# Performance work log

Measured on AMD Instinct MI355X. Metric: run time of the kernel, lower is better.

The kernel has to match this reference:

```python
import jax, jax.numpy as jnp
import numpy as np

N, F, H, C, K = 4096, 128, 128, 10, 4  # nodes, feat dim, hidden, classes, num_graphs
EDGE_P = 0.005


def setup_inputs() -> dict:
    key = jax.random.key(0)
    ks = jax.random.split(key, 20)
    feat_matrix = jax.random.normal(ks[0], (N, F), jnp.float32)
    # binary adjacency (dense_to_sparse + GCNConv without edge_weight => weights all 1)
    adj = (jax.random.uniform(ks[1], (N, N, K)) < EDGE_P).astype(jnp.float32)
    adj_matrix = adj * (1.0 - jnp.eye(N, dtype=jnp.float32))[:, :, None]  # no self loops in input
    s = 0.05
    gcn_w1 = jax.random.normal(ks[2], (K, F, H), jnp.float32) * s
    gcn_b1 = jnp.zeros((K, H), jnp.float32)
    gcn_w2 = jax.random.normal(ks[3], (K, H, H), jnp.float32) * s
    gcn_b2 = jnp.zeros((K, H), jnp.float32)
    # PyTorch LSTM params (gate order i,f,g,o), forward and backward directions
    wih_f = jax.random.normal(ks[4], (4 * H, H), jnp.float32) * s
    whh_f = jax.random.normal(ks[5], (4 * H, H), jnp.float32) * s
    bih_f = jnp.zeros((4 * H,), jnp.float32)
    bhh_f = jnp.zeros((4 * H,), jnp.float32)
    wih_b = jax.random.normal(ks[6], (4 * H, H), jnp.float32) * s
    whh_b = jax.random.normal(ks[7], (4 * H, H), jnp.float32) * s
    bih_b = jnp.zeros((4 * H,), jnp.float32)
    bhh_b = jnp.zeros((4 * H,), jnp.float32)
    rnn_out_w = jax.random.normal(ks[8], (1, 2 * H), jnp.float32) * s
    rnn_out_b = jnp.zeros((1,), jnp.float32)
    out_w = jax.random.normal(ks[9], (C, H), jnp.float32) * s
    out_b = jnp.zeros((C,), jnp.float32)
    get_item_index = jnp.arange(N, dtype=jnp.int64)
    set_index = jax.random.randint(ks[10], (1024,), 0, N).astype(jnp.int64)
    val_index = jax.random.randint(ks[11], (1024,), 0, N).astype(jnp.int64)
    mask_matrix = jnp.ones((N,), jnp.bool_)
    return dict(feat_matrix=feat_matrix, adj_matrix=adj_matrix,
                gcn_w1=gcn_w1, gcn_b1=gcn_b1, gcn_w2=gcn_w2, gcn_b2=gcn_b2,
                wih_f=wih_f, whh_f=whh_f, bih_f=bih_f, bhh_f=bhh_f,
                wih_b=wih_b, whh_b=whh_b, bih_b=bih_b, bhh_b=bhh_b,
                rnn_out_w=rnn_out_w, rnn_out_b=rnn_out_b, out_w=out_w, out_b=out_b,
                get_item_index=get_item_index, set_index=set_index,
                val_index=val_index, mask_matrix=mask_matrix)


def _gcn_norm(adj):
    # GCNConv default: A_hat = A + I, sym-normalized D^-1/2 A_hat D^-1/2
    a_hat = adj + jnp.eye(adj.shape[0], dtype=adj.dtype)
    dinv = jax.lax.rsqrt(a_hat.sum(axis=1))
    return dinv[:, None] * a_hat * dinv[None, :]


def _lstm_dir(xs, wih, whh, bih, bhh, reverse):
    # xs: [N, K, H] -> hs: [N, K, H]; scan over the (short) block axis K
    n, h = xs.shape[0], whh.shape[1]
    def step(carry, x_t):
        hp, cp = carry
        g = x_t @ wih.T + hp @ whh.T + (bih + bhh)
        i, f, gg, o = jnp.split(g, 4, axis=-1)
        c = jax.nn.sigmoid(f) * cp + jax.nn.sigmoid(i) * jnp.tanh(gg)
        hn = jax.nn.sigmoid(o) * jnp.tanh(c)
        return (hn, c), hn
    init = (jnp.zeros((n, h), xs.dtype), jnp.zeros((n, h), xs.dtype))
    _, hs = jax.lax.scan(step, init, jnp.swapaxes(xs, 0, 1), reverse=reverse)
    return jnp.swapaxes(hs, 0, 1)


def reference(feat_matrix, adj_matrix, gcn_w1, gcn_b1, gcn_w2, gcn_b2,
              wih_f, whh_f, bih_f, bhh_f, wih_b, whh_b, bih_b, bhh_b,
              rnn_out_w, rnn_out_b, out_w, out_b,
              get_item_index, set_index, val_index, mask_matrix):
    k_blocks = adj_matrix.shape[-1]
    gnn_output = []
    for k in range(k_blocks):  # fixed small number of structurally distinct graph blocks
        an = _gcn_norm(adj_matrix[:, :, k])                 # [N, N]
        h = an @ (feat_matrix @ gcn_w1[k]) + gcn_b1[k]      # GCNConv 1 (no activation)
        h = an @ (h @ gcn_w2[k]) + gcn_b2[k]                # GCNConv 2
        gnn_output.append(h)
    gnn_out = jnp.stack(gnn_output, axis=1)                 # [N, K, H]
    h_fwd = _lstm_dir(gnn_out, wih_f, whh_f, bih_f, bhh_f, reverse=False)
    h_bwd = _lstm_dir(gnn_out, wih_b, whh_b, bih_b, bhh_b, reverse=True)
    rnn_hid = jnp.concatenate([h_fwd, h_bwd], axis=-1)      # [N, K, 2H]
    attn = jax.nn.softmax(rnn_hid @ rnn_out_w.T + rnn_out_b, axis=1)  # [N, K, 1]
    pooled = (gnn_out * attn).sum(axis=1)                   # [N, H]
    return jax.nn.softmax(pooled @ out_w.T + out_b, axis=-1)  # [N, C]
```

## Files before the change

kernel.cpp:

```cpp
#include <hip/hip_runtime.h>
#include <hip/hip_bf16.h>

#define NN 4096
#define HD 128
#define KG 4
#define NC 10
#define CAP 64

typedef __attribute__((ext_vector_type(8))) short bf16x8;
typedef __attribute__((ext_vector_type(4))) float f32x4;

__device__ inline unsigned short f2b(float x) {
    unsigned u = __float_as_uint(x);
    return (unsigned short)((u + 0x7FFFu + ((u >> 16) & 1u)) >> 16);
}
__device__ inline uint2 pack4(float4 v) {
    uint2 p;
    p.x = (unsigned)f2b(v.x) | ((unsigned)f2b(v.y) << 16);
    p.y = (unsigned)f2b(v.z) | ((unsigned)f2b(v.w) << 16);
    return p;
}

__global__ __launch_bounds__(256) void prep_kernel(
    const float* __restrict__ wih_f, const float* __restrict__ whh_f,
    const float* __restrict__ bih_f, const float* __restrict__ bhh_f,
    const float* __restrict__ wih_b, const float* __restrict__ whh_b,
    const float* __restrict__ bih_b, const float* __restrict__ bhh_b,
    const float* __restrict__ gw1, const float* __restrict__ gw2,
    unsigned short* __restrict__ Wp, float* __restrict__ bp,
    unsigned short* __restrict__ Wg1p, unsigned short* __restrict__ Wg2p)
{
    int tid = blockIdx.x * 256 + threadIdx.x;
    if (tid < 2 * 512 * 256) {
        int dir = tid >> 17;
        int rem = tid & 131071;
        int n = rem >> 8, k = rem & 255;
        int tn = n >> 7, wn = (n >> 6) & 1, g = (n >> 4) & 3, c = n & 15;
        int h = tn * 32 + wn * 16 + c;
        int row = g * HD + h;
        const float* wih = dir ? wih_b : wih_f;
        const float* whh = dir ? whh_b : whh_f;
        float v = (k < HD) ? wih[row * HD + k] : whh[row * HD + (k - HD)];
        Wp[tid] = f2b(v);
    } else if (tid < 2 * 512 * 256 + 512 * 128) {
        int t = tid - 2 * 512 * 256;
        int n = t >> 7, k = t & 127;
        int kg = n >> 7, hcol = n & 127;
        Wg1p[t] = f2b(gw1[((size_t)kg * HD + k) * HD + hcol]);
    } else if (tid < 2 * 512 * 256 + 2 * 512 * 128) {
        int t = tid - (2 * 512 * 256 + 512 * 128);
        int n = t >> 7, k = t & 127;
        int kg = n >> 7, hcol = n & 127;
        Wg2p[t] = f2b(gw2[((size_t)kg * HD + k) * HD + hcol]);
    }
    if (tid < 2 * 512) {
        int dir = tid >> 9, n = tid & 511;
        int tn = n >> 7, wn = (n >> 6) & 1, g = (n >> 4) & 3, c = n & 15;
        int h = tn * 32 + wn * 16 + c;
        int row = g * HD + h;
        const float* bih = dir ? bih_b : bih_f;
        const float* bhh = dir ? bhh_b : bhh_f;
        bp[tid] = bih[row] + bhh[row];
    }
}

__global__ __launch_bounds__(256) void extract_kernel(
    const float* __restrict__ adj, float* __restrict__ dinv,
    int* __restrict__ ecnt, unsigned short* __restrict__ edges)
{
    int i = blockIdx.x;
    __shared__ int cnt[KG];
    if (threadIdx.x < KG) cnt[threadIdx.x] = 0;
    __syncthreads();
    const float4* row = (const float4*)(adj + (size_t)i * NN * KG);
    for (int j = threadIdx.x; j < NN; j += 256) {
        float4 v = row[j];
        if (v.x != 0.f) { int p = atomicAdd(&cnt[0], 1); if (p < CAP) edges[((size_t)(0 * NN + i)) * CAP + p] = (unsigned short)j; }
        if (v.y != 0.f) { int p = atomicAdd(&cnt[1], 1); if (p < CAP) edges[((size_t)(1 * NN + i)) * CAP + p] = (unsigned short)j; }
        if (v.z != 0.f) { int p = atomicAdd(&cnt[2], 1); if (p < CAP) edges[((size_t)(2 * NN + i)) * CAP + p] = (unsigned short)j; }
        if (v.w != 0.f) { int p = atomicAdd(&cnt[3], 1); if (p < CAP) edges[((size_t)(3 * NN + i)) * CAP + p] = (unsigned short)j; }
    }
    __syncthreads();
    if (threadIdx.x < KG) {
        int c = cnt[threadIdx.x];
        ecnt[threadIdx.x * NN + i] = c > CAP ? CAP : c;
        dinv[threadIdx.x * NN + i] = rsqrtf((float)c + 1.0f);
    }
}

__device__ inline void stageA(const float* __restrict__ A, int lda, int m0, int kc,
                              unsigned short* Abuf)
{
    int t = threadIdx.x;
#pragma unroll
    for (int it = 0; it < 2; ++it) {
        int f = t + it * 256;
        int r = f >> 3, q = f & 7;
        float4 v = *(const float4*)(A + (size_t)(m0 + r) * lda + kc + (q << 2));
        *(uint2*)&Abuf[r * 40 + q * 4] = pack4(v);
    }
}
__device__ inline void stageB(const unsigned short* __restrict__ Bp, int ldk,
                              int bn0, int kc, unsigned short* Bbuf)
{
    int t = threadIdx.x;
#pragma unroll
    for (int it = 0; it < 2; ++it) {
        int f = t + it * 256;
        int r = f >> 2, q = f & 3;
        uint4 v = *(const uint4*)(Bp + (size_t)(bn0 + r) * ldk + kc + (q << 3));
        *(uint4*)&Bbuf[r * 40 + q * 8] = v;
    }
}
__device__ inline void mfma_chunk(const unsigned short* Abuf, const unsigned short* Bbuf,
                                  int wm, int wn, int lane, f32x4 acc[2][4])
{
    int la = lane & 15, kb = (lane >> 4) * 8;
    bf16x8 a[2], b[4];
#pragma unroll
    for (int m = 0; m < 2; ++m)
        a[m] = *(const bf16x8*)&Abuf[(wm * 32 + m * 16 + la) * 40 + kb];
#pragma unroll
    for (int n = 0; n < 4; ++n)
        b[n] = *(const bf16x8*)&Bbuf[(wn * 64 + n * 16 + la) * 40 + kb];
#pragma unroll
    for (int m = 0; m < 2; ++m)
#pragma unroll
        for (int n = 0; n < 4; ++n)
            acc[m][n] = __builtin_amdgcn_mfma_f32_16x16x32_bf16(a[m], b[n], acc[m][n], 0, 0, 0);
}

__global__ __launch_bounds__(256) void gemm_gcn_mfma(
    const float* __restrict__ Aall, int a_per_k,
    const unsigned short* __restrict__ Bp, float* __restrict__ C)
{
    __shared__ unsigned short Abuf[64 * 40];
    __shared__ unsigned short Bbuf[128 * 40];
    int kg = blockIdx.x;
    int m0 = blockIdx.y * 64;
    const float* A = Aall + (a_per_k ? (size_t)kg * NN * HD : 0);
    int wid = threadIdx.x >> 6, lane = threadIdx.x & 63;
    int wm = wid >> 1, wn = wid & 1;
    f32x4 acc[2][4] = {};
    for (int ch = 0; ch < 4; ++ch) {
        stageA(A, HD, m0, ch * 32, Abuf);
        stageB(Bp, HD, kg * 128, ch * 32, Bbuf);
        __syncthreads();
        mfma_chunk(Abuf, Bbuf, wm, wn, lane, acc);
        __syncthreads();
    }
    float* Cb = C + (size_t)kg * NN * HD;
    int la = lane & 15, lj = lane >> 4;
#pragma unroll
    for (int m = 0; m < 2; ++m)
#pragma unroll
        for (int n = 0; n < 4; ++n)
#pragma unroll
            for (int j = 0; j < 4; ++j) {
                int r = m0 + wm * 32 + m * 16 + lj * 4 + j;
                int col = wn * 64 + n * 16 + la;
                Cb[(size_t)r * HD + col] = acc[m][n][j];
            }
}

__global__ __launch_bounds__(256) void spmm_kernel(
    const float* __restrict__ Z, const float* __restrict__ dinv,
    const int* __restrict__ ecnt, const unsigned short* __restrict__ edges,
    const float* __restrict__ bias, float* __restrict__ Out)
{
    int wid = threadIdx.x >> 6;
    int lane = threadIdx.x & 63;
    int idx = blockIdx.x * 4 + wid;
    int k = idx >> 12;
    int i = idx & (NN - 1);
    int cnt = ecnt[idx];
    float di = dinv[idx];
    const unsigned short* el = edges + (size_t)idx * CAP;
    const float* Zk = Z + (size_t)k * NN * HD;
    int h2 = lane * 2;
    float ax = 0.f, ay = 0.f;
    for (int e = 0; e < cnt; ++e) {
        int j = el[e];
        float dj = dinv[(k << 12) + j];
        float2 z = *(const float2*)(Zk + (size_t)j * HD + h2);
        ax = fmaf(dj, z.x, ax);
        ay = fmaf(dj, z.y, ay);
    }
    float2 zi = *(const float2*)(Zk + (size_t)i * HD + h2);
    ax = fmaf(di, zi.x, ax);
    ay = fmaf(di, zi.y, ay);
    float2 b = *(const float2*)(bias + k * HD + h2);
    float2 o;
    o.x = fmaf(di, ax, b.x);
    o.y = fmaf(di, ay, b.y);
    *(float2*)(Out + (size_t)idx * HD + h2) = o;
}

template <int FIRST>
__global__ __launch_bounds__(256) void lstm_step_mfma(
    const float* __restrict__ gnn, float* __restrict__ hs,
    float* __restrict__ cstate, const unsigned short* __restrict__ Wp,
    const float* __restrict__ bp, int t)
{
    __shared__ unsigned short Abuf[64 * 40];
    __shared__ unsigned short Bbuf[128 * 40];
    int dir = blockIdx.z;
    int kin   = (dir == 0) ? t : (KG - 1 - t);
    int kprev = (dir == 0) ? (t - 1) : (KG - t);
    int bn0 = blockIdx.x * 128;
    int m0  = blockIdx.y * 64;
    int wid = threadIdx.x >> 6, lane = threadIdx.x & 63;
    int wm = wid >> 1, wn = wid & 1;
    const unsigned short* B = Wp + (size_t)dir * 512 * 256;
    const float* A1 = gnn + (size_t)kin * NN * HD;
    const float* A2 = FIRST ? A1 : hs + ((size_t)dir * KG + kprev) * NN * HD;
    f32x4 acc[2][4] = {};
    int nch = FIRST ? 4 : 8;
    for (int ch = 0; ch < nch; ++ch) {
        const float* A = (ch < 4) ? A1 : A2;
        stageA(A, HD, m0, (ch & 3) * 32, Abuf);
        stageB(B, 256, bn0, ch * 32, Bbuf);
        __syncthreads();
        mfma_chunk(Abuf, Bbuf, wm, wn, lane, acc);
        __syncthreads();
    }
    int la = lane & 15, lj = lane >> 4;
    int h = blockIdx.x * 32 + wn * 16 + la;
    const float* bpd = bp + dir * 512;
    float bi = bpd[bn0 + wn * 64 + 0 * 16 + la];
    float bf = bpd[bn0 + wn * 64 + 1 * 16 + la];
    float bg = bpd[bn0 + wn * 64 + 2 * 16 + la];
    float bo = bpd[bn0 + wn * 64 + 3 * 16 + la];
    float* hout = hs + ((size_t)dir * KG + kin) * NN * HD;
    float* cst = cstate + (size_t)dir * NN * HD;
#pragma unroll
    for (int m = 0; m < 2; ++m)
#pragma unroll
        for (int j = 0; j < 4; ++j) {
            int n = m0 + wm * 32 + m * 16 + lj * 4 + j;
            float gi = acc[m][0][j] + bi;
            float gf = acc[m][1][j] + bf;
            float gg = acc[m][2][j] + bg;
            float go = acc[m][3][j] + bo;
            float cold = FIRST ? 0.f : cst[(size_t)n * HD + h];
            float si = 1.f / (1.f + __expf(-gi));
            float sf = 1.f / (1.f + __expf(-gf));
            float so = 1.f / (1.f + __expf(-go));
            float e2g = __expf(2.f * gg);
            float tg = 1.f - 2.f / (e2g + 1.f);
            float cn = fmaf(sf, cold, si * tg);
            float e2c = __expf(2.f * cn);
            float tc = 1.f - 2.f / (e2c + 1.f);
            cst[(size_t)n * HD + h] = cn;
            hout[(size_t)n * HD + h] = so * tc;
        }
}

__global__ __launch_bounds__(256) void finalize_kernel(
    const float* __restrict__ gnn, const float* __restrict__ hs,
    const float* __restrict__ rw, const float* __restrict__ ow,
    const float* __restrict__ ob, float* __restrict__ out)
{
    int wid = threadIdx.x >> 6, lane = threadIdx.x & 63;
    int n = blockIdx.x * 4 + wid;
    float w0 = rw[lane], w1 = rw[lane + 64];
    float w2 = rw[128 + lane], w3 = rw[192 + lane];
    float lg[KG];
#pragma unroll
    for (int k = 0; k < KG; ++k) {
        const float* hf = hs + ((size_t)k * NN + n) * HD;
        const float* hb = hs + ((size_t)(KG + k) * NN + n) * HD;
        lg[k] = hf[lane] * w0 + hf[lane + 64] * w1 + hb[lane] * w2 + hb[lane + 64] * w3;
    }
#pragma unroll
    for (int s = 32; s > 0; s >>= 1)
#pragma unroll
        for (int k = 0; k < KG; ++k) lg[k] += __shfl_xor(lg[k], s);
    float mx = lg[0];
#pragma unroll
    for (int k = 1; k < KG; ++k) mx = fmaxf(mx, lg[k]);
    float es[KG], se = 0.f;
#pragma unroll
    for (int k = 0; k < KG; ++k) { es[k] = __expf(lg[k] - mx); se += es[k]; }
    float inv = 1.f / se;
    float p0 = 0.f, p1 = 0.f;
#pragma unroll
    for (int k = 0; k < KG; ++k) {
        float a = es[k] * inv;
        p0 = fmaf(a, gnn[((size_t)k * NN + n) * HD + lane], p0);
        p1 = fmaf(a, gnn[((size_t)k * NN + n) * HD + lane + 64], p1);
    }
    float oc[NC];
#pragma unroll
    for (int c = 0; c < NC; ++c)
        oc[c] = p0 * ow[c * HD + lane] + p1 * ow[c * HD + lane + 64];
#pragma unroll
    for (int s = 32; s > 0; s >>= 1)
#pragma unroll
        for (int c = 0; c < NC; ++c) oc[c] += __shfl_xor(oc[c], s);
    float omx = oc[0] + ob[0];
#pragma unroll
    for (int c = 0; c < NC; ++c) { oc[c] += ob[c]; omx = fmaxf(omx, oc[c]); }
    float osum = 0.f;
#pragma unroll
    for (int c = 0; c < NC; ++c) { oc[c] = __expf(oc[c] - omx); osum += oc[c]; }
    float oinv = 1.f / osum;
    if (lane < NC) out[(size_t)n * NC + lane] = oc[lane] * oinv;
}

extern "C" void kernel_launch(void* const* d_in, const int* in_sizes, int n_in,
                              void* d_out, int out_size, void* d_ws, size_t ws_size,
                              hipStream_t stream)
{
    const float* feat  = (const float*)d_in[0];
    const float* adj   = (const float*)d_in[1];
    const float* gw1   = (const float*)d_in[2];
    const float* gb1   = (const float*)d_in[3];
    const float* gw2   = (const float*)d_in[4];
    const float* gb2   = (const float*)d_in[5];
    const float* wih_f = (const float*)d_in[6];
    const float* whh_f = (const float*)d_in[7];
    const float* bih_f = (const float*)d_in[8];
    const float* bhh_f = (const float*)d_in[9];
    const float* wih_b = (const float*)d_in[10];
    const float* whh_b = (const float*)d_in[11];
    const float* bih_b = (const float*)d_in[12];
    const float* bhh_b = (const float*)d_in[13];
    const float* rw    = (const float*)d_in[14];
    const float* ow    = (const float*)d_in[16];
    const float* ob    = (const float*)d_in[17];
    float* out = (float*)d_out;

    char* ws = (char*)d_ws;
    float*          dinv  = (float*)(ws);
    int*            ecnt  = (int*)(ws + 65536);
    unsigned short* edges = (unsigned short*)(ws + 131072);
    float*          Z     = (float*)(ws + 2228224);
    float*          G     = (float*)(ws + 10616832);
    float*          hsb   = (float*)(ws + 19005440);
    float*          cst   = (float*)(ws + 35782656);
    unsigned short* Wp    = (unsigned short*)(ws + 39976960);
    float*          bp    = (float*)(ws + 40501248);
    unsigned short* Wg1p  = (unsigned short*)(ws + 40505344);
    unsigned short* Wg2p  = (unsigned short*)(ws + 40636416);

    prep_kernel<<<1536, 256, 0, stream>>>(wih_f, whh_f, bih_f, bhh_f,
                                          wih_b, whh_b, bih_b, bhh_b,
                                          gw1, gw2, Wp, bp, Wg1p, Wg2p);
    extract_kernel<<<NN, 256, 0, stream>>>(adj, dinv, ecnt, edges);
    gemm_gcn_mfma<<<dim3(KG, 64), 256, 0, stream>>>(feat, 0, Wg1p, Z);
    spmm_kernel<<<KG * NN / 4, 256, 0, stream>>>(Z, dinv, ecnt, edges, gb1, G);
    gemm_gcn_mfma<<<dim3(KG, 64), 256, 0, stream>>>(G, 1, Wg2p, Z);
    spmm_kernel<<<KG * NN / 4, 256, 0, stream>>>(Z, dinv, ecnt, edges, gb2, G);
    lstm_step_mfma<1><<<dim3(4, 64, 2), 256, 0, stream>>>(G, hsb, cst, Wp, bp, 0);
    for (int t = 1; t < KG; ++t)
        lstm_step_mfma<0><<<dim3(4, 64, 2), 256, 0, stream>>>(G, hsb, cst, Wp, bp, t);
    finalize_kernel<<<NN / 4, 256, 0, stream>>>(G, hsb, rw, ow, ob, out);
}
```

Before: 548.3 us.

## Fuse setup kernels, emit bf16 intermediates, and fuse LSTM timesteps into one kernel

Merges the prep and adjacency-extraction kernels into one setup launch that also converts features to bf16. The SpMM now writes bf16 copies of its output, so the GEMMs and LSTM load bf16 directly without converting in the inner loop. The four per-timestep LSTM launches become one persistent kernel that keeps the cell state in registers and h in LDS, removing the global c/h round trips and the extra launches. The trade-off is that the LSTM runs on only 128 blocks with a large LDS footprint, and hidden states are stored in bf16, which costs precision.

```diff
diff --git a/kernel.cpp b/kernel.cpp
--- a/kernel.cpp
+++ b/kernel.cpp
@@ -14,143 +14,116 @@
     unsigned u = __float_as_uint(x);
     return (unsigned short)((u + 0x7FFFu + ((u >> 16) & 1u)) >> 16);
 }
-__device__ inline uint2 pack4(float4 v) {
-    uint2 p;
-    p.x = (unsigned)f2b(v.x) | ((unsigned)f2b(v.y) << 16);
-    p.y = (unsigned)f2b(v.z) | ((unsigned)f2b(v.w) << 16);
-    return p;
-}
-
-__global__ __launch_bounds__(256) void prep_kernel(
+__device__ inline float b2f(unsigned short b) {
+    return __uint_as_float((unsigned)b << 16);
+}
+
+__global__ __launch_bounds__(256) void setup_kernel(
+    const float* __restrict__ adj, const float* __restrict__ feat,
     const float* __restrict__ wih_f, const float* __restrict__ whh_f,
     const float* __restrict__ bih_f, const float* __restrict__ bhh_f,
     const float* __restrict__ wih_b, const float* __restrict__ whh_b,
     const float* __restrict__ bih_b, const float* __restrict__ bhh_b,
     const float* __restrict__ gw1, const float* __restrict__ gw2,
+    float* __restrict__ dinv, int* __restrict__ ecnt,
+    unsigned short* __restrict__ edges, unsigned* __restrict__ featb,
     unsigned short* __restrict__ Wp, float* __restrict__ bp,
     unsigned short* __restrict__ Wg1p, unsigned short* __restrict__ Wg2p)
 {
-    int tid = blockIdx.x * 256 + threadIdx.x;
-    if (tid < 2 * 512 * 256) {
-        int dir = tid >> 17;
-        int rem = tid & 131071;
+    int b = blockIdx.x;
+    __shared__ int cnt[KG];
+    if (b < NN) {
+        int i = b;
+        if (threadIdx.x < KG) cnt[threadIdx.x] = 0;
+        __syncthreads();
+        const float4* row = (const float4*)(adj + (size_t)i * NN * KG);
+        for (int j = threadIdx.x; j < NN; j += 256) {
+            float4 v = row[j];
+            if (v.x != 0.f) { int p = atomicAdd(&cnt[0], 1); if (p < CAP) edges[((size_t)(0 * NN + i)) * CAP + p] = (unsigned short)j; }
+            if (v.y != 0.f) { int p = atomicAdd(&cnt[1], 1); if (p < CAP) edges[((size_t)(1 * NN + i)) * CAP + p] = (unsigned short)j; }
+            if (v.z != 0.f) { int p = atomicAdd(&cnt[2], 1); if (p < CAP) edges[((size_t)(2 * NN + i)) * CAP + p] = (unsigned short)j; }
+            if (v.w != 0.f) { int p = atomicAdd(&cnt[3], 1); if (p < CAP) edges[((size_t)(3 * NN + i)) * CAP + p] = (unsigned short)j; }
+        }
+        __syncthreads();
+        if (threadIdx.x < KG) {
+            int c = cnt[threadIdx.x];
+            ecnt[threadIdx.x * NN + i] = c > CAP ? CAP : c;
+            dinv[threadIdx.x * NN + i] = rsqrtf((float)c + 1.0f);
+        }
+    } else if (b < NN + 1024) {
+        int t = (b - NN) * 256 + threadIdx.x;
+        int dir = t >> 17, rem = t & 131071;
         int n = rem >> 8, k = rem & 255;
-        int tn = n >> 7, wn = (n >> 6) & 1, g = (n >> 4) & 3, c = n & 15;
-        int h = tn * 32 + wn * 16 + c;
-        int row = g * HD + h;
+        int hq = n >> 6, g = (n >> 4) & 3, hr = n & 15;
+        int row = g * HD + hq * 16 + hr;
         const float* wih = dir ? wih_b : wih_f;
         const float* whh = dir ? whh_b : whh_f;
-        float v = (k < HD) ? wih[row * HD + k] : whh[row * HD + (k - HD)];
-        Wp[tid] = f2b(v);
-    } else if (tid < 2 * 512 * 256 + 512 * 128) {
-        int t = tid - 2 * 512 * 256;
+        Wp[t] = f2b(k < HD ? wih[row * HD + k] : whh[row * HD + (k - HD)]);
+    } else if (b < NN + 1280) {
+        int t = (b - NN - 1024) * 256 + threadIdx.x;
         int n = t >> 7, k = t & 127;
-        int kg = n >> 7, hcol = n & 127;
-        Wg1p[t] = f2b(gw1[((size_t)kg * HD + k) * HD + hcol]);
-    } else if (tid < 2 * 512 * 256 + 2 * 512 * 128) {
-        int t = tid - (2 * 512 * 256 + 512 * 128);
+        Wg1p[t] = f2b(gw1[(((size_t)(n >> 7)) * HD + k) * HD + (n & 127)]);
+    } else if (b < NN + 1536) {
+        int t = (b - NN - 1280) * 256 + threadIdx.x;
         int n = t >> 7, k = t & 127;
-        int kg = n >> 7, hcol = n & 127;
-        Wg2p[t] = f2b(gw2[((size_t)kg * HD + k) * HD + hcol]);
-    }
-    if (tid < 2 * 512) {
-        int dir = tid >> 9, n = tid & 511;
-        int tn = n >> 7, wn = (n >> 6) & 1, g = (n >> 4) & 3, c = n & 15;
-        int h = tn * 32 + wn * 16 + c;
-        int row = g * HD + h;
-        const float* bih = dir ? bih_b : bih_f;
-        const float* bhh = dir ? bhh_b : bhh_f;
-        bp[tid] = bih[row] + bhh[row];
-    }
-}
-
-__global__ __launch_bounds__(256) void extract_kernel(
-    const float* __restrict__ adj, float* __restrict__ dinv,
-    int* __restrict__ ecnt, unsigned short* __restrict__ edges)
-{
-    int i = blockIdx.x;
-    __shared__ int cnt[KG];
-    if (threadIdx.x < KG) cnt[threadIdx.x] = 0;
-    __syncthreads();
-    const float4* row = (const float4*)(adj + (size_t)i * NN * KG);
-    for (int j = threadIdx.x; j < NN; j += 256) {
-        float4 v = row[j];
-        if (v.x != 0.f) { int p = atomicAdd(&cnt[0], 1); if (p < CAP) edges[((size_t)(0 * NN + i)) * CAP + p] = (unsigned short)j; }
-        if (v.y != 0.f) { int p = atomicAdd(&cnt[1], 1); if (p < CAP) edges[((size_t)(1 * NN + i)) * CAP + p] = (unsigned short)j; }
-        if (v.z != 0.f) { int p = atomicAdd(&cnt[2], 1); if (p < CAP) edges[((size_t)(2 * NN + i)) * CAP + p] = (unsigned short)j; }
-        if (v.w != 0.f) { int p = atomicAdd(&cnt[3], 1); if (p < CAP) edges[((size_t)(3 * NN + i)) * CAP + p] = (unsigned short)j; }
-    }
-    __syncthreads();
-    if (threadIdx.x < KG) {
-        int c = cnt[threadIdx.x];
-        ecnt[threadIdx.x * NN + i] = c > CAP ? CAP : c;
-        dinv[threadIdx.x * NN + i] = rsqrtf((float)c + 1.0f);
-    }
-}
-
-__device__ inline void stageA(const float* __restrict__ A, int lda, int m0, int kc,
-                              unsigned short* Abuf)
-{
-    int t = threadIdx.x;
-#pragma unroll
-    for (int it = 0; it < 2; ++it) {
-        int f = t + it * 256;
-        int r = f >> 3, q = f & 7;
-        float4 v = *(const float4*)(A + (size_t)(m0 + r) * lda + kc + (q << 2));
-        *(uint2*)&Abuf[r * 40 + q * 4] = pack4(v);
-    }
-}
-__device__ inline void stageB(const unsigned short* __restrict__ Bp, int ldk,
-                              int bn0, int kc, unsigned short* Bbuf)
-{
-    int t = threadIdx.x;
-#pragma unroll
-    for (int it = 0; it < 2; ++it) {
-        int f = t + it * 256;
-        int r = f >> 2, q = f & 3;
-        uint4 v = *(const uint4*)(Bp + (size_t)(bn0 + r) * ldk + kc + (q << 3));
-        *(uint4*)&Bbuf[r * 40 + q * 8] = v;
-    }
-}
-__device__ inline void mfma_chunk(const unsigned short* Abuf, const unsigned short* Bbuf,
-                                  int wm, int wn, int lane, f32x4 acc[2][4])
-{
-    int la = lane & 15, kb = (lane >> 4) * 8;
-    bf16x8 a[2], b[4];
-#pragma unroll
-    for (int m = 0; m < 2; ++m)
-        a[m] = *(const bf16x8*)&Abuf[(wm * 32 + m * 16 + la) * 40 + kb];
-#pragma unroll
-    for (int n = 0; n < 4; ++n)
-        b[n] = *(const bf16x8*)&Bbuf[(wn * 64 + n * 16 + la) * 40 + kb];
-#pragma unroll
-    for (int m = 0; m < 2; ++m)
-#pragma unroll
-        for (int n = 0; n < 4; ++n)
-            acc[m][n] = __builtin_amdgcn_mfma_f32_16x16x32_bf16(a[m], b[n], acc[m][n], 0, 0, 0);
+        Wg2p[t] = f2b(gw2[(((size_t)(n >> 7)) * HD + k) * HD + (n & 127)]);
+    } else if (b < NN + 2560) {
+        int t = (b - NN - 1536) * 256 + threadIdx.x;
+        float2 v = *(const float2*)&feat[2 * (size_t)t];
+        featb[t] = (unsigned)f2b(v.x) | ((unsigned)f2b(v.y) << 16);
+    } else {
+        int t = (b - NN - 2560) * 256 + threadIdx.x;
+        if (t < 1024) {
+            int dir = t >> 9, n = t & 511;
+            int hq = n >> 6, g = (n >> 4) & 3, hr = n & 15;
+            int row = g * HD + hq * 16 + hr;
+            bp[t] = dir ? (bih_b[row] + bhh_b[row]) : (bih_f[row] + bhh_f[row]);
+        }
+    }
 }
 
 __global__ __launch_bounds__(256) void gemm_gcn_mfma(
-    const float* __restrict__ Aall, int a_per_k,
+    const unsigned short* __restrict__ Ab, int a_per_k,
     const unsigned short* __restrict__ Bp, float* __restrict__ C)
 {
     __shared__ unsigned short Abuf[64 * 40];
     __shared__ unsigned short Bbuf[128 * 40];
-    int kg = blockIdx.x;
-    int m0 = blockIdx.y * 64;
-    const float* A = Aall + (a_per_k ? (size_t)kg * NN * HD : 0);
+    int kg = blockIdx.x, m0 = blockIdx.y * 64;
+    const unsigned short* A = Ab + (a_per_k ? (size_t)kg * NN * HD : 0);
     int wid = threadIdx.x >> 6, lane = threadIdx.x & 63;
     int wm = wid >> 1, wn = wid & 1;
+    int la = lane & 15, kb = (lane >> 4) * 8;
     f32x4 acc[2][4] = {};
     for (int ch = 0; ch < 4; ++ch) {
-        stageA(A, HD, m0, ch * 32, Abuf);
-        stageB(Bp, HD, kg * 128, ch * 32, Bbuf);
-        __syncthreads();
-        mfma_chunk(Abuf, Bbuf, wm, wn, lane, acc);
+        {
+            int t = threadIdx.x, r = t >> 2, q = t & 3;
+            *(uint4*)&Abuf[r * 40 + q * 8] =
+                *(const uint4*)&A[((size_t)(m0 + r)) * HD + ch * 32 + q * 8];
+        }
+#pragma unroll
+        for (int it = 0; it < 2; ++it) {
+            int f = threadIdx.x + it * 256;
+            int r = f >> 2, q = f & 3;
+            *(uint4*)&Bbuf[r * 40 + q * 8] =
+                *(const uint4*)&Bp[((size_t)(kg * 128 + r)) * HD + ch * 32 + q * 8];
+        }
+        __syncthreads();
+        bf16x8 a[2], bb[4];
+#pragma unroll
+        for (int m = 0; m < 2; ++m)
+            a[m] = *(const bf16x8*)&Abuf[(wm * 32 + m * 16 + la) * 40 + kb];
+#pragma unroll
+        for (int n = 0; n < 4; ++n)
+            bb[n] = *(const bf16x8*)&Bbuf[(wn * 64 + n * 16 + la) * 40 + kb];
+#pragma unroll
+        for (int m = 0; m < 2; ++m)
+#pragma unroll
+            for (int n = 0; n < 4; ++n)
+                acc[m][n] = __builtin_amdgcn_mfma_f32_16x16x32_bf16(a[m], bb[n], acc[m][n], 0, 0, 0);
         __syncthreads();
     }
     float* Cb = C + (size_t)kg * NN * HD;
-    int la = lane & 15, lj = lane >> 4;
+    int lj = lane >> 4;
 #pragma unroll
     for (int m = 0; m < 2; ++m)
 #pragma unroll
@@ -163,10 +136,12 @@
             }
 }
 
+template <int WF32>
 __global__ __launch_bounds__(256) void spmm_kernel(
     const float* __restrict__ Z, const float* __restrict__ dinv,
     const int* __restrict__ ecnt, const unsigned short* __restrict__ edges,
-    const float* __restrict__ bias, float* __restrict__ Out)
+    const float* __restrict__ bias, float* __restrict__ Out,
+    unsigned* __restrict__ Outb)
 {
     int wid = threadIdx.x >> 6;
     int lane = threadIdx.x & 63;
@@ -189,88 +164,116 @@
     float2 zi = *(const float2*)(Zk + (size_t)i * HD + h2);
     ax = fmaf(di, zi.x, ax);
     ay = fmaf(di, zi.y, ay);
-    float2 b = *(const float2*)(bias + k * HD + h2);
+    float2 bv = *(const float2*)(bias + k * HD + h2);
     float2 o;
-    o.x = fmaf(di, ax, b.x);
-    o.y = fmaf(di, ay, b.y);
-    *(float2*)(Out + (size_t)idx * HD + h2) = o;
-}
-
-template <int FIRST>
-__global__ __launch_bounds__(256) void lstm_step_mfma(
-    const float* __restrict__ gnn, float* __restrict__ hs,
-    float* __restrict__ cstate, const unsigned short* __restrict__ Wp,
-    const float* __restrict__ bp, int t)
-{
+    o.x = fmaf(di, ax, bv.x);
+    o.y = fmaf(di, ay, bv.y);
+    if (WF32) *(float2*)(Out + (size_t)idx * HD + h2) = o;
+    Outb[(size_t)idx * 64 + lane] = (unsigned)f2b(o.x) | ((unsigned)f2b(o.y) << 16);
+}
+
+__global__ __launch_bounds__(256) void lstm_fused(
+    const unsigned short* __restrict__ G2b, unsigned short* __restrict__ hsb,
+    const unsigned short* __restrict__ Wp, const float* __restrict__ bp)
+{
+    __shared__ unsigned short Bbuf[512 * 40];
     __shared__ unsigned short Abuf[64 * 40];
-    __shared__ unsigned short Bbuf[128 * 40];
-    int dir = blockIdx.z;
-    int kin   = (dir == 0) ? t : (KG - 1 - t);
-    int kprev = (dir == 0) ? (t - 1) : (KG - t);
-    int bn0 = blockIdx.x * 128;
-    int m0  = blockIdx.y * 64;
+    __shared__ unsigned short hlds[64 * 136];
+    int m0 = blockIdx.x * 64;
+    int dir = blockIdx.y;
     int wid = threadIdx.x >> 6, lane = threadIdx.x & 63;
-    int wm = wid >> 1, wn = wid & 1;
+    int la = lane & 15, lj = lane >> 4, kb = lj * 8;
     const unsigned short* B = Wp + (size_t)dir * 512 * 256;
-    const float* A1 = gnn + (size_t)kin * NN * HD;
-    const float* A2 = FIRST ? A1 : hs + ((size_t)dir * KG + kprev) * NN * HD;
-    f32x4 acc[2][4] = {};
-    int nch = FIRST ? 4 : 8;
-    for (int ch = 0; ch < nch; ++ch) {
-        const float* A = (ch < 4) ? A1 : A2;
-        stageA(A, HD, m0, (ch & 3) * 32, Abuf);
-        stageB(B, 256, bn0, ch * 32, Bbuf);
-        __syncthreads();
-        mfma_chunk(Abuf, Bbuf, wm, wn, lane, acc);
-        __syncthreads();
-    }
-    int la = lane & 15, lj = lane >> 4;
-    int h = blockIdx.x * 32 + wn * 16 + la;
-    const float* bpd = bp + dir * 512;
-    float bi = bpd[bn0 + wn * 64 + 0 * 16 + la];
-    float bf = bpd[bn0 + wn * 64 + 1 * 16 + la];
-    float bg = bpd[bn0 + wn * 64 + 2 * 16 + la];
-    float bo = bpd[bn0 + wn * 64 + 3 * 16 + la];
-    float* hout = hs + ((size_t)dir * KG + kin) * NN * HD;
-    float* cst = cstate + (size_t)dir * NN * HD;
-#pragma unroll
-    for (int m = 0; m < 2; ++m)
-#pragma unroll
-        for (int j = 0; j < 4; ++j) {
-            int n = m0 + wm * 32 + m * 16 + lj * 4 + j;
-            float gi = acc[m][0][j] + bi;
-            float gf = acc[m][1][j] + bf;
-            float gg = acc[m][2][j] + bg;
-            float go = acc[m][3][j] + bo;
-            float cold = FIRST ? 0.f : cst[(size_t)n * HD + h];
-            float si = 1.f / (1.f + __expf(-gi));
-            float sf = 1.f / (1.f + __expf(-gf));
-            float so = 1.f / (1.f + __expf(-go));
-            float e2g = __expf(2.f * gg);
-            float tg = 1.f - 2.f / (e2g + 1.f);
-            float cn = fmaf(sf, cold, si * tg);
-            float e2c = __expf(2.f * cn);
-            float tc = 1.f - 2.f / (e2c + 1.f);
-            cst[(size_t)n * HD + h] = cn;
-            hout[(size_t)n * HD + h] = so * tc;
-        }
+    float c_st[4][2][4] = {};
+    float bias[2][4];
+#pragma unroll
+    for (int ch = 0; ch < 2; ++ch)
+#pragma unroll
+        for (int g = 0; g < 4; ++g)
+            bias[ch][g] = bp[dir * 512 + wid * 128 + (ch * 4 + g) * 16 + la];
+
+    for (int t = 0; t < KG; ++t) {
+        int kin = dir ? (KG - 1 - t) : t;
+        f32x4 acc[4][8] = {};
+        int nch = (t == 0) ? 4 : 8;
+        for (int ch = 0; ch < nch; ++ch) {
+            if (ch < 4) {
+                int r = threadIdx.x >> 2, q = threadIdx.x & 3;
+                *(uint4*)&Abuf[r * 40 + q * 8] =
+                    *(const uint4*)&G2b[((size_t)kin * NN + m0 + r) * HD + ch * 32 + q * 8];
+            }
+#pragma unroll
+            for (int it = 0; it < 8; ++it) {
+                int f = threadIdx.x + it * 256;
+                int r = f >> 2, q = f & 3;
+                *(uint4*)&Bbuf[r * 40 + q * 8] =
+                    *(const uint4*)&B[(size_t)r * 256 + ch * 32 + q * 8];
+            }
+            __syncthreads();
+            bf16x8 bfr[8];
+#pragma unroll
+            for (int fi = 0; fi < 8; ++fi)
+                bfr[fi] = *(const bf16x8*)&Bbuf[(wid * 128 + fi * 16 + la) * 40 + kb];
+#pragma unroll
+            for (int m = 0; m < 4; ++m) {
+                bf16x8 afr = (ch < 4)
+                    ? *(const bf16x8*)&Abuf[(m * 16 + la) * 40 + kb]
+                    : *(const bf16x8*)&hlds[(m * 16 + la) * 136 + (ch - 4) * 32 + kb];
+#pragma unroll
+                for (int fi = 0; fi < 8; ++fi)
+                    acc[m][fi] = __builtin_amdgcn_mfma_f32_16x16x32_bf16(afr, bfr[fi], acc[m][fi], 0, 0, 0);
+            }
+            __syncthreads();
+        }
+        unsigned short* hout = hsb + ((size_t)(dir * KG + kin) * NN) * HD;
+#pragma unroll
+        for (int m = 0; m < 4; ++m)
+#pragma unroll
+            for (int j = 0; j < 4; ++j) {
+                int r = m * 16 + lj * 4 + j;
+#pragma unroll
+                for (int chf = 0; chf < 2; ++chf) {
+                    int h = wid * 32 + chf * 16 + la;
+                    float gi = acc[m][chf * 4 + 0][j] + bias[chf][0];
+                    float gf = acc[m][chf * 4 + 1][j] + bias[chf][1];
+                    float gg = acc[m][chf * 4 + 2][j] + bias[chf][2];
+                    float go = acc[m][chf * 4 + 3][j] + bias[chf][3];
+                    float cold = c_st[m][chf][j];
+                    float si = 1.f / (1.f + __expf(-gi));
+                    float sf = 1.f / (1.f + __expf(-gf));
+                    float so = 1.f / (1.f + __expf(-go));
+                    float e2g = __expf(2.f * gg);
+                    float tg = 1.f - 2.f / (e2g + 1.f);
+                    float cn = fmaf(sf, cold, si * tg);
+                    float e2c = __expf(2.f * cn);
+                    float tc = 1.f - 2.f / (e2c + 1.f);
+                    c_st[m][chf][j] = cn;
+                    unsigned short hb = f2b(so * tc);
+                    hlds[r * 136 + h] = hb;
+                    hout[(size_t)(m0 + r) * HD + h] = hb;
+                }
+            }
+        __syncthreads();
+    }
 }
 
 __global__ __launch_bounds__(256) void finalize_kernel(
-    const float* __restrict__ gnn, const float* __restrict__ hs,
+    const float* __restrict__ gnn, const unsigned* __restrict__ hsu,
     const float* __restrict__ rw, const float* __restrict__ ow,
     const float* __restrict__ ob, float* __restrict__ out)
 {
     int wid = threadIdx.x >> 6, lane = threadIdx.x & 63;
     int n = blockIdx.x * 4 + wid;
-    float w0 = rw[lane], w1 = rw[lane + 64];
-    float w2 = rw[128 + lane], w3 = rw[192 + lane];
+    int u0 = 2 * lane;
+    float w0 = rw[u0], w1 = rw[u0 + 1];
+    float w2 = rw[HD + u0], w3 = rw[HD + u0 + 1];
     float lg[KG];
 #pragma unroll
     for (int k = 0; k < KG; ++k) {
-        const float* hf = hs + ((size_t)k * NN + n) * HD;
-        const float* hb = hs + ((size_t)(KG + k) * NN + n) * HD;
-        lg[k] = hf[lane] * w0 + hf[lane + 64] * w1 + hb[lane] * w2 + hb[lane + 64] * w3;
+        unsigned hf = hsu[((size_t)k * NN + n) * 64 + lane];
+        unsigned hb = hsu[((size_t)(KG + k) * NN + n) * 64 + lane];
+        lg[k] = b2f((unsigned short)hf) * w0 + b2f((unsigned short)(hf >> 16)) * w1
+              + b2f((unsigned short)hb) * w2 + b2f((unsigned short)(hb >> 16)) * w3;
     }
 #pragma unroll
     for (int s = 32; s > 0; s >>= 1)
@@ -287,13 +290,14 @@
 #pragma unroll
     for (int k = 0; k < KG; ++k) {
         float a = es[k] * inv;
-        p0 = fmaf(a, gnn[((size_t)k * NN + n) * HD + lane], p0);
-        p1 = fmaf(a, gnn[((size_t)k * NN + n) * HD + lane + 64], p1);
+        float2 g = *(const float2*)(gnn + ((size_t)k * NN + n) * HD + u0);
+        p0 = fmaf(a, g.x, p0);
+        p1 = fmaf(a, g.y, p1);
     }
     float oc[NC];
 #pragma unroll
     for (int c = 0; c < NC; ++c)
-        oc[c] = p0 * ow[c * HD + lane] + p1 * ow[c * HD + lane + 64];
+        oc[c] = p0 * ow[c * HD + u0] + p1 * ow[c * HD + u0 + 1];
 #pragma unroll
     for (int s = 32; s > 0; s >>= 1)
 #pragma unroll
@@ -335,25 +339,24 @@
     float*          dinv  = (float*)(ws);
     int*            ecnt  = (int*)(ws + 65536);
     unsigned short* edges = (unsigned short*)(ws + 131072);
-    float*          Z     = (float*)(ws + 2228224);
-    float*          G     = (float*)(ws + 10616832);
-    float*          hsb   = (float*)(ws + 19005440);
-    float*          cst   = (float*)(ws + 35782656);
-    unsigned short* Wp    = (unsigned short*)(ws + 39976960);
-    float*          bp    = (float*)(ws + 40501248);
-    unsigned short* Wg1p  = (unsigned short*)(ws + 40505344);
-    unsigned short* Wg2p  = (unsigned short*)(ws + 40636416);
-
-    prep_kernel<<<1536, 256, 0, stream>>>(wih_f, whh_f, bih_f, bhh_f,
-                                          wih_b, whh_b, bih_b, bhh_b,
-                                          gw1, gw2, Wp, bp, Wg1p, Wg2p);
-    extract_kernel<<<NN, 256, 0, stream>>>(adj, dinv, ecnt, edges);
-    gemm_gcn_mfma<<<dim3(KG, 64), 256, 0, stream>>>(feat, 0, Wg1p, Z);
-    spmm_kernel<<<KG * NN / 4, 256, 0, stream>>>(Z, dinv, ecnt, edges, gb1, G);
-    gemm_gcn_mfma<<<dim3(KG, 64), 256, 0, stream>>>(G, 1, Wg2p, Z);
-    spmm_kernel<<<KG * NN / 4, 256, 0, stream>>>(Z, dinv, ecnt, edges, gb2, G);
-    lstm_step_mfma<1><<<dim3(4, 64, 2), 256, 0, stream>>>(G, hsb, cst, Wp, bp, 0);
-    for (int t = 1; t < KG; ++t)
-        lstm_step_mfma<0><<<dim3(4, 64, 2), 256, 0, stream>>>(G, hsb, cst, Wp, bp, t);
-    finalize_kernel<<<NN / 4, 256, 0, stream>>>(G, hsb, rw, ow, ob, out);
-}
+    unsigned*       featb = (unsigned*)(ws + 2228224);
+    float*          Z     = (float*)(ws + 3276800);
+    unsigned*       G1b   = (unsigned*)(ws + 11665408);
+    float*          G2    = (float*)(ws + 15859712);
+    unsigned*       G2b   = (unsigned*)(ws + 24248320);
+    unsigned short* hsb   = (unsigned short*)(ws + 28442624);
+    unsigned short* Wp    = (unsigned short*)(ws + 36831232);
+    float*          bp    = (float*)(ws + 37355520);
+    unsigned short* Wg1p  = (unsigned short*)(ws + 37359616);
+    unsigned short* Wg2p  = (unsigned short*)(ws + 37490688);
+
+    setup_kernel<<<NN + 2564, 256, 0, stream>>>(
+        adj, feat, wih_f, whh_f, bih_f, bhh_f, wih_b, whh_b, bih_b, bhh_b,
+        gw1, gw2, dinv, ecnt, edges, featb, Wp, bp, Wg1p, Wg2p);
+    gemm_gcn_mfma<<<dim3(KG, 64), 256, 0, stream>>>((const unsigned short*)featb, 0, Wg1p, Z);
+    spmm_kernel<0><<<KG * NN / 4, 256, 0, stream>>>(Z, dinv, ecnt, edges, gb1, nullptr, G1b);
+    gemm_gcn_mfma<<<dim3(KG, 64), 256, 0, stream>>>((const unsigned short*)G1b, 1, Wg2p, Z);
+    spmm_kernel<1><<<KG * NN / 4, 256, 0, stream>>>(Z, dinv, ecnt, edges, gb2, G2, G2b);
+    lstm_fused<<<dim3(64, 2), 256, 0, stream>>>((const unsigned short*)G2b, hsb, Wp, bp);
+    finalize_kernel<<<NN / 4, 256, 0, stream>>>(G2, (const unsigned*)hsb, rw, ow, ob, out);
+}
```

Result: no change. 544.2 us (-0.7%).
